# Optimization experiments

Hardware: AMD Instinct MI355X
Metric: run time of the kernel (lower is better)

## Reference

```python
import jax, jax.numpy as jnp
import numpy as np

INPUT_DIM = 512
HIDDEN_DIM = 512
NUM_HEADS = 8
HEAD_DIM = HIDDEN_DIM // NUM_HEADS


def setup_inputs() -> dict:
    key = jax.random.key(0)
    ks = jax.random.split(key, 9)
    B, S = 4, 2048
    s_in = 1.0 / np.sqrt(INPUT_DIM)
    s_h = 1.0 / np.sqrt(HIDDEN_DIM)
    return {
        "x": jax.random.normal(ks[0], (B, S, INPUT_DIM), dtype=jnp.float32),
        "Wq": jax.random.uniform(ks[1], (INPUT_DIM, HIDDEN_DIM), jnp.float32, -s_in, s_in),
        "bq": jax.random.uniform(ks[2], (HIDDEN_DIM,), jnp.float32, -s_in, s_in),
        "Wk": jax.random.uniform(ks[3], (INPUT_DIM, HIDDEN_DIM), jnp.float32, -s_in, s_in),
        "bk": jax.random.uniform(ks[4], (HIDDEN_DIM,), jnp.float32, -s_in, s_in),
        "Wv": jax.random.uniform(ks[5], (INPUT_DIM, HIDDEN_DIM), jnp.float32, -s_in, s_in),
        "bv": jax.random.uniform(ks[6], (HIDDEN_DIM,), jnp.float32, -s_in, s_in),
        "Wo": jax.random.uniform(ks[7], (HIDDEN_DIM, HIDDEN_DIM), jnp.float32, -s_h, s_h),
        "bo": jax.random.uniform(ks[8], (HIDDEN_DIM,), jnp.float32, -s_h, s_h),
    }


def reference(x, Wq, bq, Wk, bk, Wv, bv, Wo, bo):
    B, S, _ = x.shape
    H, D = NUM_HEADS, HEAD_DIM
    # separate QKV projections
    q = (x @ Wq + bq).reshape(B, S, H, D)
    k = (x @ Wk + bk).reshape(B, S, H, D)
    v = (x @ Wv + bv).reshape(B, S, H, D)
    # scaled dot-product attention (non-causal, full matrix as in source)
    scores = jnp.einsum("bqhd,bkhd->bhqk", q, k) / jnp.sqrt(jnp.float32(D))
    probs = jax.nn.softmax(scores, axis=-1)
    out = jnp.einsum("bhqk,bkhd->bqhd", probs, v).reshape(B, S, H * D)
    return out @ Wo + bo
```

## Files before the change

kernel.cpp:

```cpp
#include <hip/hip_runtime.h>
#include <stdint.h>

#define B_   4
#define S_   2048
#define IN_  512
#define HID_ 512
#define NH_  8
#define HD_  64
#define M_   (B_*S_)

typedef __attribute__((ext_vector_type(8)))  short  short8;
typedef __attribute__((ext_vector_type(4)))  short  short4v;
typedef __attribute__((ext_vector_type(4)))  float  f32x4;
typedef __attribute__((ext_vector_type(16))) float  f32x16;
typedef __attribute__((ext_vector_type(8)))  __bf16 bf16x8;
typedef __attribute__((ext_vector_type(2)))  __bf16 bf16x2;
typedef __attribute__((ext_vector_type(4)))  unsigned int u32x4;
typedef __attribute__((ext_vector_type(2)))  unsigned int u32x2;

__device__ __forceinline__ unsigned short f2bf(float f) {
  union { float f; unsigned u; } v; v.f = f;
  unsigned r = (v.u + 0x7fffu + ((v.u >> 16) & 1u)) >> 16;
  return (unsigned short)r;
}

__device__ __forceinline__ unsigned int packbf(float a, float b) {
  bf16x2 t; t[0] = (__bf16)a; t[1] = (__bf16)b;
  return __builtin_bit_cast(unsigned int, t);
}

__device__ __forceinline__ u32x2 pl32swap(unsigned int a, unsigned int b) {
  return __builtin_amdgcn_permlane32_swap(a, b, false, false);
}

__device__ __forceinline__ f32x4 mfma_bf16(short8 a, short8 b, f32x4 c) {
  return __builtin_amdgcn_mfma_f32_16x16x32_bf16(
      __builtin_bit_cast(bf16x8, a), __builtin_bit_cast(bf16x8, b), c, 0, 0, 0);
}

__device__ __forceinline__ f32x16 mfma32(short8 a, short8 b, f32x16 c) {
  return __builtin_amdgcn_mfma_f32_32x32x16_bf16(
      __builtin_bit_cast(bf16x8, a), __builtin_bit_cast(bf16x8, b), c, 0, 0, 0);
}

__device__ __forceinline__ void gload_lds16(const void* g, void* l) {
  __builtin_amdgcn_global_load_lds(
      (__attribute__((address_space(1))) void*)g,
      (__attribute__((address_space(3))) void*)l, 16, 0, 0);
}

__global__ __launch_bounds__(256) void sa_prep(const float* __restrict__ x,
                                               short* __restrict__ xb,
                                               const float* __restrict__ Wq,
                                               const float* __restrict__ Wk,
                                               const float* __restrict__ Wv,
                                               const float* __restrict__ Wo,
                                               short* __restrict__ Wt) {
  __shared__ float tile[32][33];
  const int bid = blockIdx.x, tid = threadIdx.x;
  if (bid < 2048) {
    int i = (bid * 256 + tid) * 8;
    const float4* p = (const float4*)&x[i];
    float4 a = p[0], b2 = p[1];
    short8 r;
    r[0] = (short)f2bf(a.x);  r[1] = (short)f2bf(a.y);
    r[2] = (short)f2bf(a.z);  r[3] = (short)f2bf(a.w);
    r[4] = (short)f2bf(b2.x); r[5] = (short)f2bf(b2.y);
    r[6] = (short)f2bf(b2.z); r[7] = (short)f2bf(b2.w);
    *(short8*)&xb[i] = r;
  } else {
    const int wb = bid - 2048;
    const int z = wb >> 8, rem = wb & 255;
    const float* src = (z == 0) ? Wq : (z == 1) ? Wk : (z == 2) ? Wv : Wo;
    const int k0 = (rem >> 4) * 32, n0 = (rem & 15) * 32;
    const int tx = tid & 31, ty = tid >> 5;
    #pragma unroll
    for (int i = 0; i < 32; i += 8)
      tile[ty + i][tx] = src[(size_t)(k0 + ty + i) * 512 + n0 + tx];
    __syncthreads();
    short* dst = Wt + (size_t)z * 262144;
    #pragma unroll
    for (int i = 0; i < 32; i += 8)
      dst[(size_t)(n0 + ty + i) * 512 + k0 + tx] = (short)f2bf(tile[tx][ty + i]);
  }
}

template <int MODE>
__global__ __launch_bounds__(256) void sa_gemm(const short* __restrict__ Abuf,
                                               const short* __restrict__ Wt,
                                               const float* __restrict__ bias0,
                                               const float* __restrict__ bias1,
                                               const float* __restrict__ bias2,
                                               short* __restrict__ Qb,
                                               short* __restrict__ Kb2,
                                               short* __restrict__ Vb2,
                                               float* __restrict__ outp) {
  __shared__ __align__(16) short A_lds[128 * 64];
  __shared__ __align__(16) short B_lds[128 * 64];
  const int tid = threadIdx.x, lane = tid & 63, wave = tid >> 6;
  const int dd0 = blockIdx.x;
  const int L = (MODE == 0) ? ((dd0 & 7) * 96 + (dd0 >> 3))
                            : ((dd0 & 7) * 32 + (dd0 >> 3));
  const int by = L & 3, bx = (L >> 2) & 63;
  const int z = (MODE == 0) ? (L >> 8) : 3;
  const int row0 = bx * 128, col0 = by * 128;
  const short* Bsrc = Wt + (size_t)z * 262144;
  const int wr = wave >> 1, wc = wave & 1;

  f32x4 acc[4][4];
  const f32x4 zf = {0.f, 0.f, 0.f, 0.f};
  #pragma unroll
  for (int mi = 0; mi < 4; ++mi)
    #pragma unroll
    for (int ni = 0; ni < 4; ++ni) acc[mi][ni] = zf;

  for (int k0 = 0; k0 < 512; k0 += 64) {
    __syncthreads();
    #pragma unroll
    for (int j = 0; j < 4; ++j) {
      int chunk = j * 256 + wave * 64 + lane;
      int row = chunk >> 3;
      int cc = (chunk & 7) ^ (row & 7);
      gload_lds16(Abuf + (size_t)(row0 + row) * 512 + k0 + cc * 8,
                  &A_lds[(j * 256 + wave * 64) * 8]);
      gload_lds16(Bsrc + (size_t)(col0 + row) * 512 + k0 + cc * 8,
                  &B_lds[(j * 256 + wave * 64) * 8]);
    }
    __syncthreads();
    #pragma unroll
    for (int kk = 0; kk < 2; ++kk) {
      short8 af[4], bf[4];
      #pragma unroll
      for (int mi = 0; mi < 4; ++mi) {
        int r = wr * 64 + mi * 16 + (lane & 15);
        int cs = (kk * 4 + (lane >> 4)) ^ (r & 7);
        af[mi] = *(const short8*)&A_lds[r * 64 + cs * 8];
      }
      #pragma unroll
      for (int ni = 0; ni < 4; ++ni) {
        int r = wc * 64 + ni * 16 + (lane & 15);
        int cs = (kk * 4 + (lane >> 4)) ^ (r & 7);
        bf[ni] = *(const short8*)&B_lds[r * 64 + cs * 8];
      }
      #pragma unroll
      for (int mi = 0; mi < 4; ++mi)
        #pragma unroll
        for (int ni = 0; ni < 4; ++ni)
          acc[mi][ni] = mfma_bf16(af[mi], bf[ni], acc[mi][ni]);
    }
  }

  if (MODE == 0) {
    const float* bias = (z == 0) ? bias0 : (z == 1) ? bias1 : bias2;
    #pragma unroll
    for (int ni = 0; ni < 4; ++ni) {
      int n = col0 + wc * 64 + ni * 16 + (lane & 15);
      float bsv = bias[n];
      int hhd = n >> 6, dd = n & 63;
      #pragma unroll
      for (int mi = 0; mi < 4; ++mi) {
        int rg = row0 + wr * 64 + mi * 16 + ((lane >> 4) << 2);
        int bb = rg >> 11, ss = rg & 2047;
        size_t bhI = (size_t)(bb * NH_ + hhd);
        if (z == 0) {
          size_t base = bhI << 17;
          #pragma unroll
          for (int j = 0; j < 4; ++j)
            Qb[base + (size_t)(ss + j) * 64 + dd] = (short)f2bf(acc[mi][ni][j] + bsv);
        } else if (z == 1) {
          int c = dd >> 4, dh = (dd >> 3) & 1, e = dd & 7;
          int t = ss >> 6, half = (ss >> 5) & 1, lr = ss & 31;
          size_t g = (bhI * 32 + t) * 4096 + (size_t)(half * 4 + c) * 512 + e;
          #pragma unroll
          for (int j = 0; j < 4; ++j)
            Kb2[g + (size_t)(dh * 32 + lr + j) * 8] = (short)f2bf(acc[mi][ni][j] + bsv);
        } else {
          int dhalf = dd >> 5, lr = dd & 31;
          int t = ss >> 6, ks = ss & 63;
          int kc = ks >> 4, kh = (ks >> 3) & 1, e0 = ks & 7;
          size_t g = (bhI * 32 + t) * 4096 + (size_t)(kc * 2 + dhalf) * 512 +
                     (size_t)(kh * 32 + lr) * 8 + e0;
          short4v pk;
          #pragma unroll
          for (int j = 0; j < 4; ++j) pk[j] = (short)f2bf(acc[mi][ni][j] + bsv);
          *(short4v*)&Vb2[g] = pk;
        }
      }
    }
  } else {
    #pragma unroll
    for (int ni = 0; ni < 4; ++ni) {
      int n = col0 + wc * 64 + ni * 16 + (lane & 15);
      float bsv = bias0[n];
      #pragma unroll
      for (int mi = 0; mi < 4; ++mi) {
        int rg = row0 + wr * 64 + mi * 16 + ((lane >> 4) << 2);
        #pragma unroll
        for (int j = 0; j < 4; ++j)
          outp[(size_t)(rg + j) * 512 + n] = acc[mi][ni][j] + bsv;
      }
    }
  }
}

__global__ __launch_bounds__(512) void sa_attn(const short* __restrict__ Qb,
                                               const short* __restrict__ Kb2,
                                               const short* __restrict__ Vb2,
                                               short* __restrict__ Ob) {
  __shared__ __align__(16) short K_lds[2][2][4096];
  __shared__ __align__(16) short V_lds[2][4096];
  const int tid = threadIdx.x, lane = tid & 63, wave = tid >> 6;
  const int seg = wave >> 2, wq = wave & 3;
  const int dd0 = blockIdx.x;
  const int wg = (dd0 & 7) * 64 + (dd0 >> 3);
  const int qb = wg & 15, hb = (wg >> 4) & 7, b = wg >> 7;
  const size_t bh32 = ((size_t)(b * NH_ + hb)) * 32;
  const int q0w = qb * 128 + wq * 32;
  const int l31 = lane & 31, hh = lane >> 5, base32 = lane & 32;
  const int stid = tid & 255;
  const int lo = lane * 8;
  const int sg16 = seg * 16;

  const size_t bhq = ((size_t)(b * NH_ + hb)) << 17;
  short8 qf[4];
  #pragma unroll
  for (int c = 0; c < 4; ++c)
    qf[c] = *(const short8*)&Qb[bhq + (size_t)(q0w + l31) * 64 + c * 16 + hh * 8];

  f32x16 o0 = {}, o1 = {};
  const f32x16 FZ = {};
  float mrow = 0.f, lpart = 0.f;
  const float cf = 0.18033688011112042f;

  auto STAGE_K = [&](int sbuf, int tg) {
    const short* Ks = Kb2 + (bh32 + tg) * 4096;
    gload_lds16(Ks + (size_t)stid * 8,         &K_lds[seg][sbuf][wq * 512]);
    gload_lds16(Ks + (size_t)(256 + stid) * 8, &K_lds[seg][sbuf][2048 + wq * 512]);
  };
  auto STAGE_V = [&](int tg) {
    const short* Vs = Vb2 + (bh32 + tg) * 4096;
    gload_lds16(Vs + (size_t)stid * 8,         &V_lds[seg][wq * 512]);
    gload_lds16(Vs + (size_t)(256 + stid) * 8, &V_lds[seg][2048 + wq * 512]);
  };
  auto QK = [&](int nbuf, f32x16& s0, f32x16& s1) {
    const short* Kt = &K_lds[seg][nbuf][0];
    __builtin_amdgcn_s_setprio(1);
    {
      short8 kf0 = *(const short8*)&Kt[lo];
      short8 kf1 = *(const short8*)&Kt[4 * 512 + lo];
      s0 = mfma32(kf0, qf[0], FZ);
      s1 = mfma32(kf1, qf[0], FZ);
    }
    #pragma unroll
    for (int c = 1; c < 4; ++c) {
      short8 kf0 = *(const short8*)&Kt[c * 512 + lo];
      short8 kf1 = *(const short8*)&Kt[(4 + c) * 512 + lo];
      s0 = mfma32(kf0, qf[c], s0);
      s1 = mfma32(kf1, qf[c], s1);
    }
    __builtin_amdgcn_s_setprio(0);
  };

  auto BODY = [&](f32x16& c0, f32x16& c1, f32x16& n0, f32x16& n1, int t,
                  bool domax) {
    const int buf = t & 1, nbuf = buf ^ 1;
    STAGE_V(sg16 + t);
    if (t + 2 < 16) STAGE_K(buf, sg16 + t + 2);
    if (t + 1 < 16) QK(nbuf, n0, n1);

    if (domax) {
      float mx = c0[0];
      #pragma unroll
      for (int r = 1; r < 16; ++r) mx = fmaxf(mx, c0[r]);
      #pragma unroll
      for (int r = 0; r < 16; ++r) mx = fmaxf(mx, c1[r]);
      u32x2 mm = pl32swap(__builtin_bit_cast(unsigned int, mx),
                          __builtin_bit_cast(unsigned int, mx));
      mrow = fmaxf(__builtin_bit_cast(float, mm[0]),
                   __builtin_bit_cast(float, mm[1]));
    }

    const float mc = mrow * cf;
    float ps0 = 0.f, ps1 = 0.f, ps2 = 0.f, ps3 = 0.f;
    #pragma unroll
    for (int r = 0; r < 16; ++r) {
      float p0 = __builtin_amdgcn_exp2f(c0[r] * cf - mc);
      float p1 = __builtin_amdgcn_exp2f(c1[r] * cf - mc);
      c0[r] = p0; c1[r] = p1;
      if ((r & 3) == 0)      ps0 += p0 + p1;
      else if ((r & 3) == 1) ps1 += p0 + p1;
      else if ((r & 3) == 2) ps2 += p0 + p1;
      else                   ps3 += p0 + p1;
    }
    lpart += (ps0 + ps1) + (ps2 + ps3);

    __syncthreads();

    const short* Vt = &V_lds[seg][0];
    __builtin_amdgcn_s_setprio(1);
    #pragma unroll
    for (int kc = 0; kc < 4; ++kc) {
      const f32x16& cs = (kc < 2) ? c0 : c1;
      const int e = (kc & 1) * 8;
      unsigned int w0 = packbf(cs[e],     cs[e + 1]);
      unsigned int w1 = packbf(cs[e + 2], cs[e + 3]);
      unsigned int w2 = packbf(cs[e + 4], cs[e + 5]);
      unsigned int w3 = packbf(cs[e + 6], cs[e + 7]);
      u32x2 p02 = pl32swap(w0, w2);
      u32x2 p13 = pl32swap(w1, w3);
      u32x4 paw = {p02[0], p13[0], p02[1], p13[1]};
      short8 pa = __builtin_bit_cast(short8, paw);
      short8 vf0 = *(const short8*)&Vt[(kc * 2) * 512 + lo];
      short8 vf1 = *(const short8*)&Vt[(kc * 2 + 1) * 512 + lo];
      o0 = mfma32(pa, vf0, o0);
      o1 = mfma32(pa, vf1, o1);
    }
    __builtin_amdgcn_s_setprio(0);
    __syncthreads();
  };

  STAGE_K(0, sg16);
  STAGE_K(1, sg16 + 1);
  __syncthreads();
  f32x16 A0, A1, B0, B1;
  QK(0, A0, A1);
  __syncthreads();

  BODY(A0, A1, B0, B1, 0, true);
  #pragma unroll
  for (int tt = 0; tt < 7; ++tt) {
    BODY(B0, B1, A0, A1, 2 * tt + 1, false);
    BODY(A0, A1, B0, B1, 2 * tt + 2, false);
  }
  BODY(B0, B1, A0, A1, 15, false);

  u32x2 lp = pl32swap(__builtin_bit_cast(unsigned int, lpart),
                      __builtin_bit_cast(unsigned int, lpart));
  float lrow = __builtin_bit_cast(float, lp[0]) + __builtin_bit_cast(float, lp[1]);

  float* Ml = (float*)&V_lds[0][0];
  float* Ox = (float*)&K_lds[0][0][0];
  if (seg == 1) {
    if (lane < 32) { Ml[wq * 64 + lane] = mrow; Ml[wq * 64 + 32 + lane] = lrow; }
    float* Og = Ox + wq * 2048;
    #pragma unroll
    for (int r = 0; r < 16; ++r) {
      int qr = (r & 3) + 8 * (r >> 2) + 4 * hh;
      Og[qr * 64 + l31]      = o0[r];
      Og[qr * 64 + 32 + l31] = o1[r];
    }
  }
  __syncthreads();
  if (seg == 0) {
    float m1 = Ml[wq * 64 + l31], l1 = Ml[wq * 64 + 32 + l31];
    float M = fmaxf(mrow, m1);
    float a0 = __builtin_amdgcn_exp2f((mrow - M) * cf);
    float a1 = __builtin_amdgcn_exp2f((m1 - M) * cf);
    float inv = 1.f / (lrow * a0 + l1 * a1);
    float* Og = Ox + wq * 2048;
    #pragma unroll
    for (int r = 0; r < 16; ++r) {
      int qr = (r & 3) + 8 * (r >> 2) + 4 * hh;
      float A0b = __shfl(a0, base32 + qr);
      float A1b = __shfl(a1, base32 + qr);
      float I   = __shfl(inv, base32 + qr);
      float v0 = (o0[r] * A0b + Og[qr * 64 + l31] * A1b) * I;
      float v1 = (o1[r] * A0b + Og[qr * 64 + 32 + l31] * A1b) * I;
      size_t rowb = ((size_t)(b * S_ + q0w + qr)) * 512 + hb * 64;
      Ob[rowb + l31]      = (short)f2bf(v0);
      Ob[rowb + 32 + l31] = (short)f2bf(v1);
    }
  }
}

extern "C" void kernel_launch(void* const* d_in, const int* in_sizes, int n_in,
                              void* d_out, int out_size, void* d_ws, size_t ws_size,
                              hipStream_t stream) {
  const float* x  = (const float*)d_in[0];
  const float* Wq = (const float*)d_in[1];
  const float* bq = (const float*)d_in[2];
  const float* Wk = (const float*)d_in[3];
  const float* bk = (const float*)d_in[4];
  const float* Wv = (const float*)d_in[5];
  const float* bv = (const float*)d_in[6];
  const float* Wo = (const float*)d_in[7];
  const float* bo = (const float*)d_in[8];
  float* out = (float*)d_out;

  short* ws = (short*)d_ws;
  short* xb  = ws;
  short* Wt  = ws + 4194304;
  short* Qb  = ws + 5242880;
  short* Kb2 = ws + 9437184;
  short* Vb2 = ws + 13631488;
  short* Ob  = ws + 17825792;

  hipLaunchKernelGGL(sa_prep, dim3(3072), dim3(256), 0, stream,
                     x, xb, Wq, Wk, Wv, Wo, Wt);
  hipLaunchKernelGGL(sa_gemm<0>, dim3(768), dim3(256), 0, stream,
                     xb, Wt, bq, bk, bv, Qb, Kb2, Vb2, (float*)nullptr);
  hipLaunchKernelGGL(sa_attn, dim3(512), dim3(512), 0, stream, Qb, Kb2, Vb2, Ob);
  hipLaunchKernelGGL(sa_gemm<1>, dim3(256), dim3(256), 0, stream,
                     Ob, Wt, bo, (const float*)nullptr, (const float*)nullptr,
                     (short*)nullptr, (short*)nullptr, (short*)nullptr, out);
}
```

Baseline: 101.1 us.

## Double-buffer V tiles and replace syncthreads with counted vmcnt waits

Adds a second V buffer in LDS so the next V tile is prefetched one iteration ahead, alongside K. The full __syncthreads drains are replaced with explicit s_waitcnt vmcnt counts plus raw s_barrier, so outstanding K/V prefetches stay in flight across barriers. The next tile's QK MFMAs move after the barrier to overlap with the PV product. This doubles V LDS use, which may lower occupancy, and the hand-tuned vmcnt counts risk races if the load accounting is wrong.

```diff
diff --git a/kernel.cpp b/kernel.cpp
--- a/kernel.cpp
+++ b/kernel.cpp
@@ -208,7 +208,7 @@
                                                const short* __restrict__ Vb2,
                                                short* __restrict__ Ob) {
   __shared__ __align__(16) short K_lds[2][2][4096];
-  __shared__ __align__(16) short V_lds[2][4096];
+  __shared__ __align__(16) short V_lds[2][2][4096];
   const int tid = threadIdx.x, lane = tid & 63, wave = tid >> 6;
   const int seg = wave >> 2, wq = wave & 3;
   const int dd0 = blockIdx.x;
@@ -237,10 +237,10 @@
     gload_lds16(Ks + (size_t)stid * 8,         &K_lds[seg][sbuf][wq * 512]);
     gload_lds16(Ks + (size_t)(256 + stid) * 8, &K_lds[seg][sbuf][2048 + wq * 512]);
   };
-  auto STAGE_V = [&](int tg) {
+  auto STAGE_V = [&](int sbuf, int tg) {
     const short* Vs = Vb2 + (bh32 + tg) * 4096;
-    gload_lds16(Vs + (size_t)stid * 8,         &V_lds[seg][wq * 512]);
-    gload_lds16(Vs + (size_t)(256 + stid) * 8, &V_lds[seg][2048 + wq * 512]);
+    gload_lds16(Vs + (size_t)stid * 8,         &V_lds[seg][sbuf][wq * 512]);
+    gload_lds16(Vs + (size_t)(256 + stid) * 8, &V_lds[seg][sbuf][2048 + wq * 512]);
   };
   auto QK = [&](int nbuf, f32x16& s0, f32x16& s1) {
     const short* Kt = &K_lds[seg][nbuf][0];
@@ -263,10 +263,8 @@
 
   auto BODY = [&](f32x16& c0, f32x16& c1, f32x16& n0, f32x16& n1, int t,
                   bool domax) {
-    const int buf = t & 1, nbuf = buf ^ 1;
-    STAGE_V(sg16 + t);
-    if (t + 2 < 16) STAGE_K(buf, sg16 + t + 2);
-    if (t + 1 < 16) QK(nbuf, n0, n1);
+    if (t + 2 < 16) STAGE_K(t & 1, sg16 + t + 2);
+    if (t + 1 < 16) STAGE_V((t + 1) & 1, sg16 + t + 1);
 
     if (domax) {
       float mx = c0[0];
@@ -279,7 +277,6 @@
       mrow = fmaxf(__builtin_bit_cast(float, mm[0]),
                    __builtin_bit_cast(float, mm[1]));
     }
-
     const float mc = mrow * cf;
     float ps0 = 0.f, ps1 = 0.f, ps2 = 0.f, ps3 = 0.f;
     #pragma unroll
@@ -294,9 +291,15 @@
     }
     lpart += (ps0 + ps1) + (ps2 + ps3);
 
-    __syncthreads();
-
-    const short* Vt = &V_lds[seg][0];
+    if (t < 14)       asm volatile("s_waitcnt vmcnt(4)" ::: "memory");
+    else if (t == 14) asm volatile("s_waitcnt vmcnt(2)" ::: "memory");
+    else              asm volatile("s_waitcnt vmcnt(0)" ::: "memory");
+    __builtin_amdgcn_s_barrier();
+    __builtin_amdgcn_sched_barrier(0);
+
+    if (t + 1 < 16) QK((t + 1) & 1, n0, n1);
+
+    const short* Vt = &V_lds[seg][t & 1][0];
     __builtin_amdgcn_s_setprio(1);
     #pragma unroll
     for (int kc = 0; kc < 4; ++kc) {
@@ -316,15 +319,19 @@
       o1 = mfma32(pa, vf1, o1);
     }
     __builtin_amdgcn_s_setprio(0);
-    __syncthreads();
+
+    __builtin_amdgcn_s_barrier();
   };
 
   STAGE_K(0, sg16);
   STAGE_K(1, sg16 + 1);
-  __syncthreads();
+  STAGE_V(0, sg16);
+  asm volatile("s_waitcnt vmcnt(4)" ::: "memory");
+  __builtin_amdgcn_s_barrier();
+  __builtin_amdgcn_sched_barrier(0);
   f32x16 A0, A1, B0, B1;
   QK(0, A0, A1);
-  __syncthreads();
+  __builtin_amdgcn_s_barrier();
 
   BODY(A0, A1, B0, B1, 0, true);
   #pragma unroll
@@ -338,7 +345,7 @@
                       __builtin_bit_cast(unsigned int, lpart));
   float lrow = __builtin_bit_cast(float, lp[0]) + __builtin_bit_cast(float, lp[1]);
 
-  float* Ml = (float*)&V_lds[0][0];
+  float* Ml = (float*)&V_lds[0][0][0];
   float* Ox = (float*)&K_lds[0][0][0];
   if (seg == 1) {
     if (lane < 32) { Ml[wq * 64 + lane] = mrow; Ml[wq * 64 + 32 + lane] = lrow; }
```

New measurement: 98.02 us. 1.03x faster.
